# Performance work log

Measured on AMD Instinct MI355X. Metric: run time of the kernel, lower is better.

The kernel has to match this reference:

```python
import jax, jax.numpy as jnp
import numpy as np

B, A, D = 2048, 256, 8
FA, FB, FP = 64, 16, 256


def setup_inputs() -> dict:
    key = jax.random.key(0)
    k1, k2, k3, k4, k5 = jax.random.split(key, 5)
    atoms = jax.random.normal(k1, (B, A, FA), dtype=jnp.float32)
    bonds = jax.random.normal(k2, (B, A, D, FB), dtype=jnp.float32)
    # edges use -1 as padding for missing neighbors
    edges = jax.random.randint(k3, (B, A, D), -1, A, dtype=jnp.int32)
    fan_in = FA + FB
    limit = np.sqrt(6.0 / (fan_in + FP)).astype(np.float32)  # glorot_uniform
    W = jax.random.uniform(k4, (fan_in, FP), minval=-limit, maxval=limit, dtype=jnp.float32)
    b = jnp.zeros((FP,), dtype=jnp.float32)
    return {"atoms": atoms, "bonds": bonds, "edges": edges, "W": W, "b": b}


def reference(atoms, bonds, edges, W, b):
    # atom degree from edge list (-1 = padded neighbor slot)
    atom_degrees = jnp.sum((edges != -1).astype(jnp.float32), axis=-1, keepdims=True)  # [B,A,1]
    general_atom_mask = (atom_degrees != 0).astype(atoms.dtype)                        # [B,A,1]
    summed_bond_features = jnp.sum(bonds, axis=-2)                                     # [B,A,FB]
    atoms_bonds = jnp.concatenate([atoms, summed_bond_features], axis=-1)              # [B,A,FA+FB]
    # TimeDistributed Dense with relu, applied per atom
    fp_unmasked = jax.nn.relu(jnp.einsum('baf,fo->bao', atoms_bonds, W) + b)           # [B,A,FP]
    fp_masked = fp_unmasked * general_atom_mask
    return jnp.sum(fp_masked, axis=-2)                                                 # [B,FP]
```

## Files before the change

kernel.cpp:

```cpp
#include <hip/hip_runtime.h>
#include <hip/hip_bf16.h>


#define NB 2048
#define NA 256
#define ND 8
#define NFA 64
#define NFB 16
#define NF 80
#define NFP 256
#define PITCH 100
#define AH 128

#define PART_OFF    (64 * 1024)

typedef __attribute__((ext_vector_type(8))) short short8;
typedef __attribute__((ext_vector_type(4))) float f32x4;

static __device__ __forceinline__ unsigned int pk2bf(float lo, float hi) {
    __hip_bfloat162 h = __float22bfloat162_rn(float2{lo, hi});
    return *reinterpret_cast<unsigned int*>(&h);
}

static __device__ __forceinline__ unsigned short f2bf(float f) {
    unsigned int u = __float_as_uint(f);
    return (unsigned short)((u + 0x7FFFu + ((u >> 16) & 1u)) >> 16);
}

__global__ void ngf_prep_w(const float* __restrict__ W, short8* __restrict__ wfrag)
{
    const int gid  = blockIdx.x;
    const int nt   = gid / 3;
    const int ks   = gid % 3;
    const int lane = threadIdx.x;
    const int c    = nt * 16 + (lane & 15);
    short8 v;
    #pragma unroll
    for (int j = 0; j < 8; ++j) {
        const int k = ks * 32 + (lane >> 4) * 8 + j;
        float w = (k < NF) ? W[k * NFP + c] : 0.0f;
        v[j] = (short)f2bf(w);
    }
    wfrag[gid * 64 + lane] = v;
}

__launch_bounds__(256, 4)
__global__ void ngf_mfma_kernel(const float4* __restrict__ atoms4,
                                const float4* __restrict__ bonds4,
                                const int4*   __restrict__ edges4,
                                const short8* __restrict__ wfrag,
                                const float*  __restrict__ bias,
                                float* __restrict__ part)
{
    const int bid  = blockIdx.x;
    const int tid  = threadIdx.x;
    const int wave = tid >> 6;
    const int lane = tid & 63;
    const int lrow = lane & 15;
    const int lgrp = lane >> 4;

    __shared__ unsigned short X[AH * PITCH];
    __shared__ float maskf[AH];

    const size_t atomBase = (size_t)bid * AH;

    const int ba = tid >> 2;
    const int q  = tid & 3;
    const float4* bp0 = bonds4 + (atomBase + ba) * 32 + q;
    const float4* bp1 = bonds4 + (atomBase + 64 + ba) * 32 + q;

    float4 bv[16];
    #pragma unroll
    for (int d = 0; d < 8; ++d) bv[d] = bp0[d * 4];
    #pragma unroll
    for (int d = 0; d < 8; ++d) bv[8 + d] = bp1[d * 4];

    float4 av[8];
    #pragma unroll
    for (int it = 0; it < 8; ++it) {
        const int flat = it * 256 + tid;
        av[it] = atoms4[(atomBase + (flat >> 4)) * 16 + (flat & 15)];
    }

    const int ea = tid & 127;
    int4 e0 = edges4[(atomBase + ea) * 2];
    int4 e1 = edges4[(atomBase + ea) * 2 + 1];

    {
        float4 s = {0.0f, 0.0f, 0.0f, 0.0f};
        #pragma unroll
        for (int d = 0; d < 8; ++d) { s.x += bv[d].x; s.y += bv[d].y; s.z += bv[d].z; s.w += bv[d].w; }
        uint2 o; o.x = pk2bf(s.x, s.y); o.y = pk2bf(s.z, s.w);
        *(uint2*)&X[ba * PITCH + NFA + q * 4] = o;
    }
    {
        float4 s = {0.0f, 0.0f, 0.0f, 0.0f};
        #pragma unroll
        for (int d = 0; d < 8; ++d) { s.x += bv[8 + d].x; s.y += bv[8 + d].y; s.z += bv[8 + d].z; s.w += bv[8 + d].w; }
        uint2 o; o.x = pk2bf(s.x, s.y); o.y = pk2bf(s.z, s.w);
        *(uint2*)&X[(64 + ba) * PITCH + NFA + q * 4] = o;
    }
    #pragma unroll
    for (int it = 0; it < 8; ++it) {
        const int flat = it * 256 + tid;
        const int a = flat >> 4, k4 = flat & 15;
        uint2 o; o.x = pk2bf(av[it].x, av[it].y); o.y = pk2bf(av[it].z, av[it].w);
        *(uint2*)&X[a * PITCH + k4 * 4] = o;
    }
    if (tid < AH) {
        bool any = (e0.x != -1) | (e0.y != -1) | (e0.z != -1) | (e0.w != -1)
                 | (e1.x != -1) | (e1.y != -1) | (e1.z != -1) | (e1.w != -1);
        maskf[ea] = any ? 1.0f : 0.0f;
        uint4 z = {0u, 0u, 0u, 0u};
        *(uint4*)&X[ea * PITCH + 80] = z;
        *(uint4*)&X[ea * PITCH + 88] = z;
    }

    short8 bf[3][4];
    float  bia[4];
    #pragma unroll
    for (int nt = 0; nt < 4; ++nt) {
        const int ntg = wave * 4 + nt;
        bia[nt] = bias[ntg * 16 + lrow];
        #pragma unroll
        for (int ks = 0; ks < 3; ++ks)
            bf[ks][nt] = wfrag[(ntg * 3 + ks) * 64 + lane];
    }
    __syncthreads();

    float colsum[4] = {0.0f, 0.0f, 0.0f, 0.0f};
    #pragma unroll 2
    for (int s = 0; s < 8; ++s) {
        const int row = s * 16 + lrow;
        const unsigned short* xr = &X[row * PITCH + lgrp * 8];
        short8 a0 = *(const short8*)(xr);
        short8 a1 = *(const short8*)(xr + 32);
        short8 a2 = *(const short8*)(xr + 64);
        float4 m4 = *(const float4*)&maskf[s * 16 + lgrp * 4];
        #pragma unroll
        for (int nt = 0; nt < 4; ++nt) {
            f32x4 acc = {0.0f, 0.0f, 0.0f, 0.0f};
            acc = __builtin_amdgcn_mfma_f32_16x16x32_bf16(a0, bf[0][nt], acc, 0, 0, 0);
            acc = __builtin_amdgcn_mfma_f32_16x16x32_bf16(a1, bf[1][nt], acc, 0, 0, 0);
            acc = __builtin_amdgcn_mfma_f32_16x16x32_bf16(a2, bf[2][nt], acc, 0, 0, 0);
            const float bv2 = bia[nt];
            colsum[nt] += fmaxf(acc[0] + bv2, 0.0f) * m4.x
                        + fmaxf(acc[1] + bv2, 0.0f) * m4.y
                        + fmaxf(acc[2] + bv2, 0.0f) * m4.z
                        + fmaxf(acc[3] + bv2, 0.0f) * m4.w;
        }
    }

    #pragma unroll
    for (int nt = 0; nt < 4; ++nt) {
        float v = colsum[nt];
        v += __shfl_xor(v, 16, 64);
        v += __shfl_xor(v, 32, 64);
        if (lane < 16)
            part[(size_t)bid * NFP + (wave * 4 + nt) * 16 + lane] = v;
    }
}

__global__ void ngf_reduce(const float* __restrict__ part, float* __restrict__ out)
{
    const int g   = blockIdx.x * 256 + threadIdx.x;
    const int mol = g >> 8;
    const int col = g & 255;
    out[g] = part[(size_t)(2 * mol) * NFP + col] + part[(size_t)(2 * mol + 1) * NFP + col];
}

extern "C" void kernel_launch(void* const* d_in, const int* in_sizes, int n_in,
                              void* d_out, int out_size, void* d_ws, size_t ws_size,
                              hipStream_t stream) {
    const float4* atoms4 = (const float4*)d_in[0];
    const float4* bonds4 = (const float4*)d_in[1];
    const int4*   edges4 = (const int4*)d_in[2];
    const float*  W      = (const float*)d_in[3];
    const float*  bias   = (const float*)d_in[4];
    float* out = (float*)d_out;

    short8* wfrag = (short8*)d_ws;
    float*  part  = (float*)((char*)d_ws + PART_OFF);

    ngf_prep_w<<<48, 64, 0, stream>>>(W, wfrag);
    ngf_mfma_kernel<<<NB * 2, 256, 0, stream>>>(atoms4, bonds4, edges4, wfrag, bias, part);
    ngf_reduce<<<2048, 256, 0, stream>>>(part, out);
}
```

Before: 88.48 us.

## Split molecules into quarter blocks and reduce with atomics instead of a reduce kernel

Halves the atoms per block from 128 to 64, which doubles the grid to four blocks per molecule. Each block atomically adds its column sums into the zeroed output, replacing the partial buffer and the separate reduce kernel. The aim is more parallelism and less register pressure, and it drops one kernel launch plus the partial-buffer round trip. In exchange it adds a memset, float atomics whose summation order is nondeterministic, and per-block weight-fragment loads that are now amortized over fewer atoms.

```diff
diff --git a/kernel.cpp b/kernel.cpp
--- a/kernel.cpp
+++ b/kernel.cpp
@@ -10,9 +10,7 @@
 #define NF 80
 #define NFP 256
 #define PITCH 100
-#define AH 128
-
-#define PART_OFF    (64 * 1024)
+#define AH 64
 
 typedef __attribute__((ext_vector_type(8))) short short8;
 typedef __attribute__((ext_vector_type(4))) float f32x4;
@@ -50,7 +48,7 @@
                                 const int4*   __restrict__ edges4,
                                 const short8* __restrict__ wfrag,
                                 const float*  __restrict__ bias,
-                                float* __restrict__ part)
+                                float* __restrict__ out)
 {
     const int bid  = blockIdx.x;
     const int tid  = threadIdx.x;
@@ -66,25 +64,24 @@
 
     const int ba = tid >> 2;
     const int q  = tid & 3;
-    const float4* bp0 = bonds4 + (atomBase + ba) * 32 + q;
-    const float4* bp1 = bonds4 + (atomBase + 64 + ba) * 32 + q;
+    const float4* bp = bonds4 + (atomBase + ba) * 32 + q;
 
-    float4 bv[16];
+    float4 bv[8];
     #pragma unroll
-    for (int d = 0; d < 8; ++d) bv[d] = bp0[d * 4];
+    for (int d = 0; d < 8; ++d) bv[d] = bp[d * 4];
+
+    float4 av[4];
     #pragma unroll
-    for (int d = 0; d < 8; ++d) bv[8 + d] = bp1[d * 4];
-
-    float4 av[8];
-    #pragma unroll
-    for (int it = 0; it < 8; ++it) {
+    for (int it = 0; it < 4; ++it) {
         const int flat = it * 256 + tid;
         av[it] = atoms4[(atomBase + (flat >> 4)) * 16 + (flat & 15)];
     }
 
-    const int ea = tid & 127;
-    int4 e0 = edges4[(atomBase + ea) * 2];
-    int4 e1 = edges4[(atomBase + ea) * 2 + 1];
+    int4 e0, e1;
+    if (tid < AH) {
+        e0 = edges4[(atomBase + tid) * 2];
+        e1 = edges4[(atomBase + tid) * 2 + 1];
+    }
 
     {
         float4 s = {0.0f, 0.0f, 0.0f, 0.0f};
@@ -93,15 +90,8 @@
         uint2 o; o.x = pk2bf(s.x, s.y); o.y = pk2bf(s.z, s.w);
         *(uint2*)&X[ba * PITCH + NFA + q * 4] = o;
     }
-    {
-        float4 s = {0.0f, 0.0f, 0.0f, 0.0f};
-        #pragma unroll
-        for (int d = 0; d < 8; ++d) { s.x += bv[8 + d].x; s.y += bv[8 + d].y; s.z += bv[8 + d].z; s.w += bv[8 + d].w; }
-        uint2 o; o.x = pk2bf(s.x, s.y); o.y = pk2bf(s.z, s.w);
-        *(uint2*)&X[(64 + ba) * PITCH + NFA + q * 4] = o;
-    }
     #pragma unroll
-    for (int it = 0; it < 8; ++it) {
+    for (int it = 0; it < 4; ++it) {
         const int flat = it * 256 + tid;
         const int a = flat >> 4, k4 = flat & 15;
         uint2 o; o.x = pk2bf(av[it].x, av[it].y); o.y = pk2bf(av[it].z, av[it].w);
@@ -110,10 +100,10 @@
     if (tid < AH) {
         bool any = (e0.x != -1) | (e0.y != -1) | (e0.z != -1) | (e0.w != -1)
                  | (e1.x != -1) | (e1.y != -1) | (e1.z != -1) | (e1.w != -1);
-        maskf[ea] = any ? 1.0f : 0.0f;
+        maskf[tid] = any ? 1.0f : 0.0f;
         uint4 z = {0u, 0u, 0u, 0u};
-        *(uint4*)&X[ea * PITCH + 80] = z;
-        *(uint4*)&X[ea * PITCH + 88] = z;
+        *(uint4*)&X[tid * PITCH + 80] = z;
+        *(uint4*)&X[tid * PITCH + 88] = z;
     }
 
     short8 bf[3][4];
@@ -129,8 +119,8 @@
     __syncthreads();
 
     float colsum[4] = {0.0f, 0.0f, 0.0f, 0.0f};
-    #pragma unroll 2
-    for (int s = 0; s < 8; ++s) {
+    #pragma unroll
+    for (int s = 0; s < 4; ++s) {
         const int row = s * 16 + lrow;
         const unsigned short* xr = &X[row * PITCH + lgrp * 8];
         short8 a0 = *(const short8*)(xr);
@@ -151,22 +141,15 @@
         }
     }
 
+    const int mol = bid >> 2;
     #pragma unroll
     for (int nt = 0; nt < 4; ++nt) {
         float v = colsum[nt];
         v += __shfl_xor(v, 16, 64);
         v += __shfl_xor(v, 32, 64);
         if (lane < 16)
-            part[(size_t)bid * NFP + (wave * 4 + nt) * 16 + lane] = v;
+            atomicAdd(&out[(size_t)mol * NFP + (wave * 4 + nt) * 16 + lane], v);
     }
-}
-
-__global__ void ngf_reduce(const float* __restrict__ part, float* __restrict__ out)
-{
-    const int g   = blockIdx.x * 256 + threadIdx.x;
-    const int mol = g >> 8;
-    const int col = g & 255;
-    out[g] = part[(size_t)(2 * mol) * NFP + col] + part[(size_t)(2 * mol + 1) * NFP + col];
 }
 
 extern "C" void kernel_launch(void* const* d_in, const int* in_sizes, int n_in,
@@ -180,9 +163,8 @@
     float* out = (float*)d_out;
 
     short8* wfrag = (short8*)d_ws;
-    float*  part  = (float*)((char*)d_ws + PART_OFF);
 
+    hipMemsetAsync(d_out, 0, (size_t)out_size * sizeof(float), stream);
     ngf_prep_w<<<48, 64, 0, stream>>>(W, wfrag);
-    ngf_mfma_kernel<<<NB * 2, 256, 0, stream>>>(atoms4, bonds4, edges4, wfrag, bias, part);
-    ngf_reduce<<<2048, 256, 0, stream>>>(part, out);
+    ngf_mfma_kernel<<<NB * 4, 256, 0, stream>>>(atoms4, bonds4, edges4, wfrag, bias, out);
 }
```

Result: slower. 106.4 us (+20.3%).
